# Kernel optimization log

Hardware: AMD Instinct MI355X
Metric: run time of the kernel (lower is better)

Reference implementation:

```python
import jax, jax.numpy as jnp
import numpy as np

B, N, S, D = 32, 128, 64, 512
MAX_LEN = 5000


def make_pe(d_model, max_len):
    pos = np.arange(max_len, dtype=np.float32)[:, None]
    div = np.exp(np.arange(0, d_model, 2, dtype=np.float32) * (-np.log(10000.0) / d_model))
    pe = np.zeros((max_len, d_model), dtype=np.float32)
    pe[:, 0::2] = np.sin(pos * div)
    pe[:, 1::2] = np.cos(pos * div)
    return jnp.asarray(pe)


def setup_inputs() -> dict:
    key = jax.random.key(0)
    ks = jax.random.split(key, 16)
    s1 = 1.0 / np.sqrt(D)
    s2 = 1.0 / np.sqrt(2 * D)
    inp = {
        "x": jax.random.normal(ks[0], (B, N), jnp.float32),
        "timesteps": jax.random.randint(ks[1], (B,), 0, 1000),
        "fusion_feat": jax.random.normal(ks[2], (B, D), jnp.float32),
        "tar_image_feat": jax.random.normal(ks[3], (B, N, S, D), jnp.float32),
        "pe": make_pe(D, MAX_LEN),
        # torch Linear weights are [out, in]
        "Wq": jax.random.normal(ks[4], (D, D), jnp.float32) * s1,
        "Wk": jax.random.normal(ks[5], (D, D), jnp.float32) * s1,
        "Wv": jax.random.normal(ks[6], (D, D), jnp.float32) * s1,
        "Wp": jax.random.normal(ks[7], (D, D), jnp.float32) * s1,
        "bp": jnp.zeros((D,), jnp.float32),
        "Wt1": jax.random.normal(ks[8], (D, D), jnp.float32) * s1,
        "bt1": jnp.zeros((D,), jnp.float32),
        "Wt2": jax.random.normal(ks[9], (D, D), jnp.float32) * s1,
        "bt2": jnp.zeros((D,), jnp.float32),
        "Wd1": jax.random.normal(ks[10], (2 * D, 2 * D), jnp.float32) * s2,
        "bd1": jnp.zeros((2 * D,), jnp.float32),
        "Wd2": jax.random.normal(ks[11], (1, 2 * D), jnp.float32) * s2,
        "bd2": jnp.zeros((1,), jnp.float32),
    }
    return inp


def reference(x, timesteps, fusion_feat, tar_image_feat, pe,
              Wq, Wk, Wv, Wp, bp, Wt1, bt1, Wt2, bt2, Wd1, bd1, Wd2, bd2):
    # timestep embedding: pe[timesteps] -> [B, D], then 2-layer SiLU MLP (eval mode: dropout off)
    cond = jax.nn.silu(pe[timesteps] @ Wt1.T + bt1) @ Wt2.T + bt2  # [B, D]

    # similarity argmax over S tokens, then gather best token per (b, n)
    sim = jnp.einsum('bd,bnsd->bns', fusion_feat, tar_image_feat)  # [B, N, S]
    best = jnp.argmax(sim, axis=-1)                                # [B, N]
    tif = jnp.take_along_axis(tar_image_feat, best[:, :, None, None], axis=2)[:, :, 0, :]  # [B, N, D]

    # single-vector attention over N candidates
    q = (fusion_feat + cond) @ Wq.T                  # [B, D]
    k = (tif + cond[:, None, :]) @ Wk.T              # [B, N, D]
    v = (tif + cond[:, None, :]) @ Wv.T              # [B, N, D]
    w = jax.nn.softmax(jnp.einsum('bd,bnd->bn', q, k) + x, axis=-1)  # [B, N]
    new_emb = jnp.einsum('bn,bnd->bd', w, v) @ Wp.T + bp             # [B, D]

    # MLP decode over concat [new_emb (broadcast), tif]
    emb = jnp.concatenate([jnp.broadcast_to(new_emb[:, None, :], tif.shape), tif], axis=-1)  # [B, N, 2D]
    h = jax.nn.relu(emb @ Wd1.T + bd1)
    p = (h @ Wd2.T + bd2)[..., 0] + w                # [B, N]

    # sort descending along N
    return -jnp.sort(-p, axis=1)
```

## Files before the change

### kernel.cpp

```cpp
#include <hip/hip_runtime.h>
#include <hip/hip_bf16.h>
#include <math.h>


#define BB 32
#define NN 128
#define SS 64
#define DD 512

typedef __attribute__((ext_vector_type(8))) short short8;
typedef __attribute__((ext_vector_type(4))) float f32x4;

__device__ __forceinline__ ushort f2bf(float f) {
    unsigned u = __float_as_uint(f);
    unsigned r = (u + 0x7fffu + ((u >> 16) & 1u)) >> 16;
    return (ushort)r;
}

__device__ __forceinline__ float wave_dot512(const float* __restrict__ w,
                                             const float* __restrict__ xl, int lane) {
    const float4* w4 = reinterpret_cast<const float4*>(w);
    const float4* x4 = reinterpret_cast<const float4*>(xl);
    float4 a0 = w4[lane * 2];
    float4 a1 = w4[lane * 2 + 1];
    float4 b0 = x4[lane * 2];
    float4 b1 = x4[lane * 2 + 1];
    float s = a0.x * b0.x + a0.y * b0.y + a0.z * b0.z + a0.w * b0.w
            + a1.x * b1.x + a1.y * b1.y + a1.z * b1.z + a1.w * b1.w;
#pragma unroll
    for (int off = 32; off; off >>= 1) s += __shfl_xor(s, off);
    return s;
}

__global__ __launch_bounds__(256) void bmv(
    const float* __restrict__ W, int ldw, const float* __restrict__ bias,
    const float* __restrict__ Xa, const float* __restrict__ Xb,
    const int* __restrict__ ts, const float* __restrict__ pe,
    float* __restrict__ Y, int R, int act, int mode) {
    __shared__ __align__(16) float xl[DD];
    int b = blockIdx.y, tid = threadIdx.x, lane = tid & 63, wave = tid >> 6;
    const float* src = (mode == 1) ? (pe + (size_t)ts[b] * DD) : (Xa + (size_t)b * DD);
    if (mode == 2) {
        const float* s2 = Xb + (size_t)b * DD;
        for (int i = tid; i < DD; i += 256) xl[i] = src[i] + s2[i];
    } else {
        for (int i = tid; i < DD; i += 256) xl[i] = src[i];
    }
    __syncthreads();
    int j0 = blockIdx.x * 16 + wave * 4;
#pragma unroll
    for (int jj = 0; jj < 4; ++jj) {
        int j = j0 + jj;
        float s = wave_dot512(W + (size_t)j * ldw, xl, lane);
        if (bias) s += bias[j];
        if (act == 1) s = s / (1.f + expf(-s));
        if (lane == 0) Y[(size_t)b * R + j] = s;
    }
}

__global__ __launch_bounds__(256) void k_qk(
    const float* __restrict__ Wk, const float* __restrict__ q,
    float* __restrict__ qk) {
    __shared__ __align__(16) float ql[DD];
    __shared__ float part[4][64];
    int b = blockIdx.y, c0 = blockIdx.x * 64;
    int tid = threadIdx.x, lane = tid & 63, wave = tid >> 6;
    for (int i = tid; i < DD; i += 256) ql[i] = q[(size_t)b * DD + i];
    __syncthreads();
    float p = 0.f;
    for (int j = wave * 128; j < wave * 128 + 128; ++j)
        p += ql[j] * Wk[(size_t)j * DD + c0 + lane];
    part[wave][lane] = p;
    __syncthreads();
    if (tid < 64)
        qk[(size_t)b * DD + c0 + tid] =
            part[0][tid] + part[1][tid] + part[2][tid] + part[3][tid];
}

__global__ __launch_bounds__(256) void k_convWb(
    const float* __restrict__ Wd1, ushort* __restrict__ Wb) {
    int i = blockIdx.x * 256 + threadIdx.x;
    int idx = i * 8;
    int r = idx >> 9, k = idx & 511;
    const float* src = Wd1 + (size_t)r * 1024 + 512 + k;
    float4 v0 = *reinterpret_cast<const float4*>(src);
    float4 v1 = *reinterpret_cast<const float4*>(src + 4);
    ushort o[8] = {f2bf(v0.x), f2bf(v0.y), f2bf(v0.z), f2bf(v0.w),
                   f2bf(v1.x), f2bf(v1.y), f2bf(v1.z), f2bf(v1.w)};
    *reinterpret_cast<short8*>(Wb + (size_t)r * 512 + k) =
        *reinterpret_cast<short8*>(o);
}

__global__ __launch_bounds__(256) void k2_sim(
    const float* __restrict__ fusion, const float* __restrict__ tif,
    const float* __restrict__ x, const float* __restrict__ qk,
    float* __restrict__ tif_best, ushort* __restrict__ abf,
    float* __restrict__ score) {
    __shared__ __align__(16) float fb[DD];
    __shared__ float bv_s[4];
    __shared__ int bi_s[4];
    __shared__ int bidx_s;
    __shared__ float dred[4];
    int bn = blockIdx.x, b = bn >> 7;
    int tid = threadIdx.x, lane = tid & 63, wave = tid >> 6;
    for (int i = tid; i < DD; i += 256) fb[i] = fusion[(size_t)b * DD + i];
    __syncthreads();
    const float* base = tif + (size_t)bn * SS * DD;
    float bv = -INFINITY;
    int bi = 0;
    for (int s = wave * 16; s < wave * 16 + 16; ++s) {
        float v = wave_dot512(base + (size_t)s * DD, fb, lane);
        if (v > bv) { bv = v; bi = s; }
    }
    if (lane == 0) { bv_s[wave] = bv; bi_s[wave] = bi; }
    __syncthreads();
    if (tid == 0) {
        float v = bv_s[0]; int i0 = bi_s[0];
        for (int w = 1; w < 4; w++)
            if (bv_s[w] > v) { v = bv_s[w]; i0 = bi_s[w]; }
        bidx_s = i0;
    }
    __syncthreads();
    const float* src = base + (size_t)bidx_s * DD;
    const float* qkb = qk + (size_t)b * DD;
    float local = 0.f;
    for (int i = tid; i < DD; i += 256) {
        float vv = src[i];
        tif_best[(size_t)bn * DD + i] = vv;
        abf[(size_t)bn * DD + i] = f2bf(vv);
        local += vv * qkb[i];
    }
#pragma unroll
    for (int off = 32; off; off >>= 1) local += __shfl_xor(local, off);
    if (lane == 0) dred[wave] = local;
    __syncthreads();
    if (tid == 0) score[bn] = dred[0] + dred[1] + dred[2] + dred[3] + x[bn];
}

__global__ __launch_bounds__(256) void k_vsum(
    const float* __restrict__ score, const float* __restrict__ tif_best,
    const float* __restrict__ cond,
    float* __restrict__ wout, float* __restrict__ vsum) {
    __shared__ float wl[NN];
    __shared__ float redm[2], reds[2];
    int b = blockIdx.y, tid = threadIdx.x, lane = tid & 63, wave = tid >> 6;
    float v = 0.f;
    if (tid < NN) {
        v = score[b * NN + tid];
        float m = v;
#pragma unroll
        for (int off = 32; off; off >>= 1) m = fmaxf(m, __shfl_xor(m, off));
        if (lane == 0) redm[wave] = m;
    }
    __syncthreads();
    float m = fmaxf(redm[0], redm[1]);
    if (tid < NN) {
        float e = expf(v - m);
        wl[tid] = e;
        float s = e;
#pragma unroll
        for (int off = 32; off; off >>= 1) s += __shfl_xor(s, off);
        if (lane == 0) reds[wave] = s;
    }
    __syncthreads();
    float inv = 1.f / (reds[0] + reds[1]);
    if (blockIdx.x == 0 && tid < NN) wout[b * NN + tid] = wl[tid] * inv;
    int d = blockIdx.x * 256 + tid;
    const float* base = tif_best + (size_t)b * NN * DD + d;
    float s = 0.f;
#pragma unroll 8
    for (int n = 0; n < NN; n++) s += wl[n] * base[(size_t)n * DD];
    vsum[(size_t)b * DD + d] = s * inv + cond[(size_t)b * DD + d];
}

__global__ __launch_bounds__(256) void k4_mfma(
    const ushort* __restrict__ Abf, const ushort* __restrict__ Wb,
    const float* __restrict__ Wd2, const float* __restrict__ u,
    float* __restrict__ p_part) {
    __shared__ ushort aS[128 * 64];
    __shared__ ushort bS[128 * 64];
    int tid = threadIdx.x, l = tid & 63, w = tid >> 6;
    int m0 = blockIdx.x * 128, n0 = blockIdx.y * 128;
    int wm = w >> 1, wn = w & 1;
    f32x4 acc[4][4];
#pragma unroll
    for (int i = 0; i < 4; i++)
#pragma unroll
        for (int j = 0; j < 4; j++) acc[i][j] = (f32x4){0.f, 0.f, 0.f, 0.f};

    for (int k0 = 0; k0 < DD; k0 += 64) {
#pragma unroll
        for (int i = 0; i < 4; ++i) {
            int L = i * 4096 + w * 1024 + l * 16;
            int row = L >> 7;
            int bo = L & 127;
            int sb = bo ^ ((row & 7) << 4);
            const ushort* ga = Abf + (size_t)(m0 + row) * DD + k0 + (sb >> 1);
            const ushort* gb = Wb + (size_t)(n0 + row) * DD + k0 + (sb >> 1);
            __builtin_amdgcn_global_load_lds(
                (const __attribute__((address_space(1))) void*)ga,
                (__attribute__((address_space(3))) void*)(aS + i * 2048 + w * 512),
                16, 0, 0);
            __builtin_amdgcn_global_load_lds(
                (const __attribute__((address_space(1))) void*)gb,
                (__attribute__((address_space(3))) void*)(bS + i * 2048 + w * 512),
                16, 0, 0);
        }
        __syncthreads();
#pragma unroll
        for (int kk = 0; kk < 2; ++kk) {
            short8 af[4], bf[4];
#pragma unroll
            for (int f = 0; f < 4; ++f) {
                int ra = wm * 64 + f * 16 + (l & 15);
                int boa = (((l >> 4) * 16 + kk * 64)) ^ ((ra & 7) << 4);
                af[f] = *reinterpret_cast<const short8*>(&aS[ra * 64 + (boa >> 1)]);
                int rb = wn * 64 + f * 16 + (l & 15);
                int bob = (((l >> 4) * 16 + kk * 64)) ^ ((rb & 7) << 4);
                bf[f] = *reinterpret_cast<const short8*>(&bS[rb * 64 + (bob >> 1)]);
            }
#pragma unroll
            for (int fm = 0; fm < 4; ++fm)
#pragma unroll
                for (int fn = 0; fn < 4; ++fn)
                    acc[fm][fn] = __builtin_amdgcn_mfma_f32_16x16x32_bf16(
                        af[fm], bf[fn], acc[fm][fn], 0, 0, 0);
        }
        __syncthreads();
    }
    int b = blockIdx.x;
    const float* ub = u + (size_t)b * 1024;
#pragma unroll
    for (int fm = 0; fm < 4; ++fm) {
#pragma unroll
        for (int reg = 0; reg < 4; ++reg) {
            float pp = 0.f;
#pragma unroll
            for (int fn = 0; fn < 4; ++fn) {
                int r = n0 + wn * 64 + fn * 16 + (l & 15);
                float h = acc[fm][fn][reg] + ub[r];
                if (h > 0.f) pp += Wd2[r] * h;
            }
#pragma unroll
            for (int off = 1; off < 16; off <<= 1) pp += __shfl_xor(pp, off);
            if ((l & 15) == 0) {
                int m = m0 + wm * 64 + fm * 16 + (l >> 4) * 4 + reg;
                p_part[(size_t)m * 16 + blockIdx.y * 2 + wn] = pp;
            }
        }
    }
}

__global__ __launch_bounds__(128) void k5_sort(
    const float* __restrict__ p_part, const float* __restrict__ wout,
    const float* __restrict__ bd2, float* __restrict__ out) {
    __shared__ float v[NN];
    int b = blockIdx.x, tid = threadIdx.x;
    int bn = b * NN + tid;
    float s = bd2[0] + wout[bn];
#pragma unroll
    for (int c = 0; c < 16; c++) s += p_part[(size_t)bn * 16 + c];
    v[tid] = s;
    __syncthreads();
    for (int k = 2; k <= NN; k <<= 1) {
        for (int j = k >> 1; j > 0; j >>= 1) {
            int ixj = tid ^ j;
            if (ixj > tid) {
                float a = v[tid], bb2 = v[ixj];
                bool desc = (tid & k) == 0;
                if (desc ? (a < bb2) : (a > bb2)) { v[tid] = bb2; v[ixj] = a; }
            }
            __syncthreads();
        }
    }
    out[bn] = v[tid];
}

extern "C" void kernel_launch(void* const* d_in, const int* in_sizes, int n_in,
                              void* d_out, int out_size, void* d_ws, size_t ws_size,
                              hipStream_t stream) {
    const float* x      = (const float*)d_in[0];
    const int*   ts     = (const int*)d_in[1];
    const float* fusion = (const float*)d_in[2];
    const float* tif    = (const float*)d_in[3];
    const float* pe     = (const float*)d_in[4];
    const float* Wq     = (const float*)d_in[5];
    const float* Wk     = (const float*)d_in[6];
    const float* Wv     = (const float*)d_in[7];
    const float* Wp     = (const float*)d_in[8];
    const float* bp     = (const float*)d_in[9];
    const float* Wt1    = (const float*)d_in[10];
    const float* bt1    = (const float*)d_in[11];
    const float* Wt2    = (const float*)d_in[12];
    const float* bt2    = (const float*)d_in[13];
    const float* Wd1    = (const float*)d_in[14];
    const float* bd1    = (const float*)d_in[15];
    const float* Wd2    = (const float*)d_in[16];
    const float* bd2    = (const float*)d_in[17];

    float* ws = (float*)d_ws;
    float* cond     = ws;
    float* qk       = cond + 16384;
    float* h        = qk + 16384;
    float* q        = h + 16384;
    float* score    = q + 16384;
    float* wout     = score + 4096;
    float* vsum     = wout + 4096;
    float* ve       = vsum + 16384;
    float* ne       = ve + 16384;
    float* u        = ne + 16384;
    float* p_part   = u + 32768;
    float* tif_best = p_part + 65536;
    ushort* Abf     = (ushort*)(tif_best + 2097152);
    ushort* Wb      = Abf + 2097152;
    float* out = (float*)d_out;

    hipLaunchKernelGGL(k_convWb, dim3(256), dim3(256), 0, stream, Wd1, Wb);
    hipLaunchKernelGGL(bmv, dim3(32, BB), dim3(256), 0, stream,
                       Wt1, DD, bt1, nullptr, nullptr, ts, pe, h, DD, 1, 1);
    hipLaunchKernelGGL(bmv, dim3(32, BB), dim3(256), 0, stream,
                       Wt2, DD, bt2, h, nullptr, nullptr, nullptr, cond, DD, 0, 0);
    hipLaunchKernelGGL(bmv, dim3(32, BB), dim3(256), 0, stream,
                       Wq, DD, nullptr, fusion, cond, nullptr, nullptr, q, DD, 0, 2);
    hipLaunchKernelGGL(k_qk, dim3(8, BB), dim3(256), 0, stream, Wk, q, qk);

    hipLaunchKernelGGL(k2_sim, dim3(BB * NN), dim3(256), 0, stream,
                       fusion, tif, x, qk, tif_best, Abf, score);

    hipLaunchKernelGGL(k_vsum, dim3(2, BB), dim3(256), 0, stream,
                       score, tif_best, cond, wout, vsum);
    hipLaunchKernelGGL(bmv, dim3(32, BB), dim3(256), 0, stream,
                       Wv, DD, nullptr, vsum, nullptr, nullptr, nullptr, ve, DD, 0, 0);
    hipLaunchKernelGGL(bmv, dim3(32, BB), dim3(256), 0, stream,
                       Wp, DD, bp, ve, nullptr, nullptr, nullptr, ne, DD, 0, 0);
    hipLaunchKernelGGL(bmv, dim3(64, BB), dim3(256), 0, stream,
                       Wd1, 2 * DD, bd1, ne, nullptr, nullptr, nullptr, u, 2 * DD, 0, 0);

    hipLaunchKernelGGL(k4_mfma, dim3(32, 8), dim3(256), 0, stream,
                       Abf, Wb, Wd2, u, p_part);
    hipLaunchKernelGGL(k5_sort, dim3(BB), dim3(128), 0, stream,
                       p_part, wout, bd2, out);
}
```

Before: 193.4 us.

## Fuse weight conversion and u-projection into existing kernels, batch row dot products

```diff
diff --git a/kernel.cpp b/kernel.cpp
--- a/kernel.cpp
+++ b/kernel.cpp
@@ -17,19 +17,24 @@
     return (ushort)r;
 }
 
-__device__ __forceinline__ float wave_dot512(const float* __restrict__ w,
-                                             const float* __restrict__ xl, int lane) {
-    const float4* w4 = reinterpret_cast<const float4*>(w);
-    const float4* x4 = reinterpret_cast<const float4*>(xl);
-    float4 a0 = w4[lane * 2];
-    float4 a1 = w4[lane * 2 + 1];
-    float4 b0 = x4[lane * 2];
-    float4 b1 = x4[lane * 2 + 1];
-    float s = a0.x * b0.x + a0.y * b0.y + a0.z * b0.z + a0.w * b0.w
-            + a1.x * b1.x + a1.y * b1.y + a1.z * b1.z + a1.w * b1.w;
-#pragma unroll
-    for (int off = 32; off; off >>= 1) s += __shfl_xor(s, off);
-    return s;
+__device__ __forceinline__ void wave_dot512x4(
+    const float* __restrict__ w, size_t ldw, float4 xa, float4 xb,
+    int lane, float out[4]) {
+    float4 ra[4], rb[4];
+#pragma unroll
+    for (int r = 0; r < 4; ++r) {
+        const float4* row = reinterpret_cast<const float4*>(w + (size_t)r * ldw);
+        ra[r] = row[lane * 2];
+        rb[r] = row[lane * 2 + 1];
+    }
+#pragma unroll
+    for (int r = 0; r < 4; ++r) {
+        float s = ra[r].x * xa.x + ra[r].y * xa.y + ra[r].z * xa.z + ra[r].w * xa.w
+                + rb[r].x * xb.x + rb[r].y * xb.y + rb[r].z * xb.z + rb[r].w * xb.w;
+#pragma unroll
+        for (int off = 32; off; off >>= 1) s += __shfl_xor(s, off);
+        out[r] = s;
+    }
 }
 
 __global__ __launch_bounds__(256) void bmv(
@@ -47,14 +52,17 @@
         for (int i = tid; i < DD; i += 256) xl[i] = src[i];
     }
     __syncthreads();
+    float4 xa = reinterpret_cast<const float4*>(xl)[lane * 2];
+    float4 xb = reinterpret_cast<const float4*>(xl)[lane * 2 + 1];
     int j0 = blockIdx.x * 16 + wave * 4;
-#pragma unroll
-    for (int jj = 0; jj < 4; ++jj) {
-        int j = j0 + jj;
-        float s = wave_dot512(W + (size_t)j * ldw, xl, lane);
-        if (bias) s += bias[j];
-        if (act == 1) s = s / (1.f + expf(-s));
-        if (lane == 0) Y[(size_t)b * R + j] = s;
+    float s[4];
+    wave_dot512x4(W + (size_t)j0 * ldw, ldw, xa, xb, lane, s);
+    if (lane < 4) {
+        int j = j0 + lane;
+        float v = s[lane];
+        if (bias) v += bias[j];
+        if (act == 1) v = v / (1.f + expf(-v));
+        Y[(size_t)b * R + j] = v;
     }
 }
 
@@ -77,23 +85,10 @@
             part[0][tid] + part[1][tid] + part[2][tid] + part[3][tid];
 }
 
-__global__ __launch_bounds__(256) void k_convWb(
-    const float* __restrict__ Wd1, ushort* __restrict__ Wb) {
-    int i = blockIdx.x * 256 + threadIdx.x;
-    int idx = i * 8;
-    int r = idx >> 9, k = idx & 511;
-    const float* src = Wd1 + (size_t)r * 1024 + 512 + k;
-    float4 v0 = *reinterpret_cast<const float4*>(src);
-    float4 v1 = *reinterpret_cast<const float4*>(src + 4);
-    ushort o[8] = {f2bf(v0.x), f2bf(v0.y), f2bf(v0.z), f2bf(v0.w),
-                   f2bf(v1.x), f2bf(v1.y), f2bf(v1.z), f2bf(v1.w)};
-    *reinterpret_cast<short8*>(Wb + (size_t)r * 512 + k) =
-        *reinterpret_cast<short8*>(o);
-}
-
 __global__ __launch_bounds__(256) void k2_sim(
     const float* __restrict__ fusion, const float* __restrict__ tif,
     const float* __restrict__ x, const float* __restrict__ qk,
+    const float* __restrict__ Wd1, ushort* __restrict__ Wb,
     float* __restrict__ tif_best, ushort* __restrict__ abf,
     float* __restrict__ score) {
     __shared__ __align__(16) float fb[DD];
@@ -103,14 +98,28 @@
     __shared__ float dred[4];
     int bn = blockIdx.x, b = bn >> 7;
     int tid = threadIdx.x, lane = tid & 63, wave = tid >> 6;
+
+    if (bn < 1024) {
+        int idx = (bn * 256 + tid) * 2;
+        int r = idx >> 9, k = idx & 511;
+        float2 v = *reinterpret_cast<const float2*>(Wd1 + (size_t)r * 1024 + 512 + k);
+        ushort2 o = {f2bf(v.x), f2bf(v.y)};
+        *reinterpret_cast<ushort2*>(Wb + (size_t)r * 512 + k) = o;
+    }
+
     for (int i = tid; i < DD; i += 256) fb[i] = fusion[(size_t)b * DD + i];
     __syncthreads();
+    float4 xa = reinterpret_cast<const float4*>(fb)[lane * 2];
+    float4 xb = reinterpret_cast<const float4*>(fb)[lane * 2 + 1];
     const float* base = tif + (size_t)bn * SS * DD;
     float bv = -INFINITY;
     int bi = 0;
-    for (int s = wave * 16; s < wave * 16 + 16; ++s) {
-        float v = wave_dot512(base + (size_t)s * DD, fb, lane);
-        if (v > bv) { bv = v; bi = s; }
+    for (int s0 = wave * 16; s0 < wave * 16 + 16; s0 += 4) {
+        float sv[4];
+        wave_dot512x4(base + (size_t)s0 * DD, DD, xa, xb, lane, sv);
+#pragma unroll
+        for (int r = 0; r < 4; ++r)
+            if (sv[r] > bv) { bv = sv[r]; bi = s0 + r; }
     }
     if (lane == 0) { bv_s[wave] = bv; bi_s[wave] = bi; }
     __syncthreads();
@@ -175,13 +184,52 @@
 
 __global__ __launch_bounds__(256) void k4_mfma(
     const ushort* __restrict__ Abf, const ushort* __restrict__ Wb,
-    const float* __restrict__ Wd2, const float* __restrict__ u,
+    const float* __restrict__ Wd1, const float* __restrict__ bd1,
+    const float* __restrict__ ne, const float* __restrict__ Wd2,
     float* __restrict__ p_part) {
     __shared__ ushort aS[128 * 64];
     __shared__ ushort bS[128 * 64];
+    __shared__ __align__(16) float nel[DD];
+    __shared__ float uloc[128];
     int tid = threadIdx.x, l = tid & 63, w = tid >> 6;
     int m0 = blockIdx.x * 128, n0 = blockIdx.y * 128;
+    int b = blockIdx.x;
     int wm = w >> 1, wn = w & 1;
+
+    for (int i = tid; i < DD; i += 256) nel[i] = ne[(size_t)b * DD + i];
+    __syncthreads();
+    float4 na = reinterpret_cast<const float4*>(nel)[l * 2];
+    float4 nb = reinterpret_cast<const float4*>(nel)[l * 2 + 1];
+
+#define STAGE(K0)                                                              \
+    {                                                                          \
+        _Pragma("unroll") for (int i = 0; i < 4; ++i) {                        \
+            int L = i * 4096 + w * 1024 + l * 16;                              \
+            int row = L >> 7;                                                  \
+            int bo = L & 127;                                                  \
+            int sb = bo ^ ((row & 7) << 4);                                    \
+            const ushort* ga = Abf + (size_t)(m0 + row) * DD + (K0) + (sb >> 1); \
+            const ushort* gb = Wb + (size_t)(n0 + row) * DD + (K0) + (sb >> 1);  \
+            __builtin_amdgcn_global_load_lds(                                  \
+                (const __attribute__((address_space(1))) void*)ga,             \
+                (__attribute__((address_space(3))) void*)(aS + i * 2048 + w * 512), \
+                16, 0, 0);                                                     \
+            __builtin_amdgcn_global_load_lds(                                  \
+                (const __attribute__((address_space(1))) void*)gb,             \
+                (__attribute__((address_space(3))) void*)(bS + i * 2048 + w * 512), \
+                16, 0, 0);                                                     \
+        }                                                                      \
+    }
+
+    STAGE(0);
+    for (int j0 = 0; j0 < 32; j0 += 4) {
+        int r = w * 32 + j0;
+        float s[4];
+        wave_dot512x4(Wd1 + (size_t)(n0 + r) * 1024, 1024, na, nb, l, s);
+        if (l < 4) uloc[r + l] = s[l] + bd1[n0 + r + l];
+    }
+    __syncthreads();
+
     f32x4 acc[4][4];
 #pragma unroll
     for (int i = 0; i < 4; i++)
@@ -189,24 +237,6 @@
         for (int j = 0; j < 4; j++) acc[i][j] = (f32x4){0.f, 0.f, 0.f, 0.f};
 
     for (int k0 = 0; k0 < DD; k0 += 64) {
-#pragma unroll
-        for (int i = 0; i < 4; ++i) {
-            int L = i * 4096 + w * 1024 + l * 16;
-            int row = L >> 7;
-            int bo = L & 127;
-            int sb = bo ^ ((row & 7) << 4);
-            const ushort* ga = Abf + (size_t)(m0 + row) * DD + k0 + (sb >> 1);
-            const ushort* gb = Wb + (size_t)(n0 + row) * DD + k0 + (sb >> 1);
-            __builtin_amdgcn_global_load_lds(
-                (const __attribute__((address_space(1))) void*)ga,
-                (__attribute__((address_space(3))) void*)(aS + i * 2048 + w * 512),
-                16, 0, 0);
-            __builtin_amdgcn_global_load_lds(
-                (const __attribute__((address_space(1))) void*)gb,
-                (__attribute__((address_space(3))) void*)(bS + i * 2048 + w * 512),
-                16, 0, 0);
-        }
-        __syncthreads();
 #pragma unroll
         for (int kk = 0; kk < 2; ++kk) {
             short8 af[4], bf[4];
@@ -227,9 +257,12 @@
                         af[fm], bf[fn], acc[fm][fn], 0, 0, 0);
         }
         __syncthreads();
-    }
-    int b = blockIdx.x;
-    const float* ub = u + (size_t)b * 1024;
+        if (k0 + 64 < DD) {
+            STAGE(k0 + 64);
+            __syncthreads();
+        }
+    }
+#undef STAGE
 #pragma unroll
     for (int fm = 0; fm < 4; ++fm) {
 #pragma unroll
@@ -237,9 +270,9 @@
             float pp = 0.f;
 #pragma unroll
             for (int fn = 0; fn < 4; ++fn) {
-                int r = n0 + wn * 64 + fn * 16 + (l & 15);
-                float h = acc[fm][fn][reg] + ub[r];
-                if (h > 0.f) pp += Wd2[r] * h;
+                int rl = wn * 64 + fn * 16 + (l & 15);
+                float hh = acc[fm][fn][reg] + uloc[rl];
+                if (hh > 0.f) pp += Wd2[n0 + rl] * hh;
             }
 #pragma unroll
             for (int off = 1; off < 16; off <<= 1) pp += __shfl_xor(pp, off);
@@ -308,14 +341,12 @@
     float* vsum     = wout + 4096;
     float* ve       = vsum + 16384;
     float* ne       = ve + 16384;
-    float* u        = ne + 16384;
-    float* p_part   = u + 32768;
+    float* p_part   = ne + 16384;
     float* tif_best = p_part + 65536;
     ushort* Abf     = (ushort*)(tif_best + 2097152);
     ushort* Wb      = Abf + 2097152;
     float* out = (float*)d_out;
 
-    hipLaunchKernelGGL(k_convWb, dim3(256), dim3(256), 0, stream, Wd1, Wb);
     hipLaunchKernelGGL(bmv, dim3(32, BB), dim3(256), 0, stream,
                        Wt1, DD, bt1, nullptr, nullptr, ts, pe, h, DD, 1, 1);
     hipLaunchKernelGGL(bmv, dim3(32, BB), dim3(256), 0, stream,
@@ -325,7 +356,7 @@
     hipLaunchKernelGGL(k_qk, dim3(8, BB), dim3(256), 0, stream, Wk, q, qk);
 
     hipLaunchKernelGGL(k2_sim, dim3(BB * NN), dim3(256), 0, stream,
-                       fusion, tif, x, qk, tif_best, Abf, score);
+                       fusion, tif, x, qk, Wd1, Wb, tif_best, Abf, score);
 
     hipLaunchKernelGGL(k_vsum, dim3(2, BB), dim3(256), 0, stream,
                        score, tif_best, cond, wout, vsum);
@@ -333,11 +364,9 @@
                        Wv, DD, nullptr, vsum, nullptr, nullptr, nullptr, ve, DD, 0, 0);
     hipLaunchKernelGGL(bmv, dim3(32, BB), dim3(256), 0, stream,
                        Wp, DD, bp, ve, nullptr, nullptr, nullptr, ne, DD, 0, 0);
-    hipLaunchKernelGGL(bmv, dim3(64, BB), dim3(256), 0, stream,
-                       Wd1, 2 * DD, bd1, ne, nullptr, nullptr, nullptr, u, 2 * DD, 0, 0);
 
     hipLaunchKernelGGL(k4_mfma, dim3(32, 8), dim3(256), 0, stream,
-                       Abf, Wb, Wd2, u, p_part);
+                       Abf, Wb, Wd1, bd1, ne, Wd2, p_part);
     hipLaunchKernelGGL(k5_sort, dim3(BB), dim3(128), 0, stream,
                        p_part, wout, bd2, out);
 }
```

After: 187.4 us. 1.03x faster.
